# Kernel optimization log

Hardware: AMD Instinct MI355X
Metric: run time of the kernel (lower is better)

The kernel has to match this reference:

```python
import jax, jax.numpy as jnp
import numpy as np

H, W, C = 56, 56, 384
WS, SHIFT, HEADS = 7, 3, 12
HEAD_DIM = C // HEADS
SCALE = HEAD_DIM ** (-0.5)
NWIN = (H // WS) * (W // WS)  # 64 windows per image
NTOK = WS * WS                # 49 tokens per window
EPS = 1e-5


def _gen_mask():
    # static shift-window attention mask, computed with numpy (jit-safe constant)
    img = np.zeros((H, W))
    sl = (slice(0, -WS), slice(-WS, -SHIFT), slice(-SHIFT, None))
    cnt = 0
    for hs in sl:
        for ws in sl:
            img[hs, ws] = cnt
            cnt += 1
    mw = img.reshape(H // WS, WS, W // WS, WS).transpose(0, 2, 1, 3).reshape(-1, NTOK)
    diff = mw[:, None, :] - mw[:, :, None]  # (NWIN, NTOK, NTOK)
    return jnp.asarray(np.where(diff != 0, -100.0, 0.0), dtype=jnp.float32)

ATTN_MASK = _gen_mask()


def _layernorm(x, g, b):
    mu = jnp.mean(x, axis=-1, keepdims=True)
    var = jnp.var(x, axis=-1, keepdims=True)
    return (x - mu) * jax.lax.rsqrt(var + EPS) * g + b


def setup_inputs() -> dict:
    key = jax.random.key(0)
    ks = jax.random.split(key, 6)
    s = 0.02
    return {
        "x": jax.random.normal(ks[0], (16, H * W, C), dtype=jnp.float32),
        "ln1_g": jnp.ones((C,), jnp.float32),
        "ln1_b": jnp.zeros((C,), jnp.float32),
        "qkv_w": jax.random.normal(ks[1], (C, 3 * C), jnp.float32) * s,
        "proj_w": jax.random.normal(ks[2], (C, C), jnp.float32) * s,
        "proj_b": jnp.zeros((C,), jnp.float32),
        "ln2_g": jnp.ones((C,), jnp.float32),
        "ln2_b": jnp.zeros((C,), jnp.float32),
        "fc1_w": jax.random.normal(ks[3], (C, 4 * C), jnp.float32) * s,
        "fc1_b": jnp.zeros((4 * C,), jnp.float32),
        "fc2_w": jax.random.normal(ks[4], (4 * C, C), jnp.float32) * s,
        "fc2_b": jnp.zeros((C,), jnp.float32),
    }


def reference(x, ln1_g, ln1_b, qkv_w, proj_w, proj_b, ln2_g, ln2_b, fc1_w, fc1_b, fc2_w, fc2_b):
    B, N, _ = x.shape
    h = x
    y = _layernorm(x, ln1_g, ln1_b).reshape(B, H, W, C)
    # cyclic shift (note: source never rolls back; we match it)
    y = jnp.roll(y, shift=(-SHIFT, -SHIFT), axis=(1, 2))
    # window partition -> (B*NWIN, NTOK, C)
    y = y.reshape(B, H // WS, WS, W // WS, WS, C).transpose(0, 1, 3, 2, 4, 5)
    y = y.reshape(B * NWIN, NTOK, C)
    # qkv (no bias), split heads
    qkv = (y @ qkv_w).reshape(B * NWIN, NTOK, 3, HEADS, HEAD_DIM)
    qkv = qkv.transpose(2, 0, 3, 1, 4)  # (3, BW, heads, NTOK, hd)
    q, k, v = qkv[0], qkv[1], qkv[2]
    attn = jnp.einsum('whnd,whmd->whnm', q, k) * SCALE  # (BW, heads, NTOK, NTOK)
    attn = attn.reshape(B, NWIN, HEADS, NTOK, NTOK) + ATTN_MASK[None, :, None]
    attn = jax.nn.softmax(attn.reshape(B * NWIN, HEADS, NTOK, NTOK), axis=-1)
    o = jnp.einsum('whnm,whmd->whnd', attn, v)
    o = o.transpose(0, 2, 1, 3).reshape(B * NWIN, NTOK, C)
    o = o @ proj_w + proj_b
    # window reverse -> (B, N, C)
    o = o.reshape(B, H // WS, W // WS, WS, WS, C).transpose(0, 1, 3, 2, 4, 5)
    o = o.reshape(B, N, C)
    x1 = h + o
    # MLP (GELU after both fc1 and fc2, as in source)
    m = _layernorm(x1, ln2_g, ln2_b)
    m = jax.nn.gelu(m @ fc1_w + fc1_b, approximate=False)
    m = jax.nn.gelu(m @ fc2_w + fc2_b, approximate=False)
    return x1 + m
```

## Files before the change

### kernel.cpp

```cpp
#include <hip/hip_runtime.h>
#include <hip/hip_bf16.h>
#include <cstdint>
#include <cstddef>

#define C_DIM   384
#define NIMG    3136
#define MROWS   50176
#define QK_SCALE 0.17677669529663687f

using bf16x8 = __attribute__((ext_vector_type(8))) short;
using f32x4  = __attribute__((ext_vector_type(4))) float;

__device__ __forceinline__ short f2bf(float f) {
  union { float f; uint32_t u; } v; v.f = f;
  uint32_t r = (v.u + 0x7fffu + ((v.u >> 16) & 1u)) >> 16;
  return (short)(uint16_t)r;
}

__device__ __forceinline__ float bf2f(short s) {
  union { uint32_t u; float f; } v; v.u = ((uint32_t)(uint16_t)s) << 16;
  return v.f;
}

__device__ __forceinline__ void async_copy16(const void* g, void* l) {
  __builtin_amdgcn_global_load_lds(
      (const __attribute__((address_space(1))) void*)g,
      (__attribute__((address_space(3))) void*)l, 16, 0, 0);
}

__device__ __forceinline__ float gelu_fast(float x) {
  float x2 = x * x;
  float u = fmaf(0.0356774081f, x2, 0.7978845608f);
  float e = exp2f(x * u * 2.8853900818f);
  float r = __builtin_amdgcn_rcpf(e + 1.0f);
  return fmaf(-x, r, x);
}

__global__ __launch_bounds__(256) void transpose_cast(
    const float* __restrict__ w, short* __restrict__ wt, int K, int N) {
  int idx = blockIdx.x * 256 + threadIdx.x;
  if (idx >= K * N) return;
  int k = idx / N;
  int n = idx - k * N;
  wt[(size_t)n * K + k] = f2bf(w[idx]);
}

template <typename IN>
__global__ __launch_bounds__(256) void ln_kernel(
    const IN* __restrict__ x, const float* __restrict__ g,
    const float* __restrict__ b, short* __restrict__ y, int windowed) {
  int token = blockIdx.x * 4 + (threadIdx.x >> 6);
  int lane = threadIdx.x & 63;
  size_t src;
  if (windowed) {
    int bw = token / 49;
    int tt = token - bw * 49;
    int bb = bw >> 6, w = bw & 63;
    int hs = (w >> 3) * 7 + tt / 7 + 3; if (hs >= 56) hs -= 56;
    int ws = (w & 7) * 7 + (tt % 7) + 3; if (ws >= 56) ws -= 56;
    src = (size_t)(bb * NIMG + hs * 56 + ws) * C_DIM;
  } else {
    src = (size_t)token * C_DIM;
  }
  const IN* xr = x + src;
  float v[6];
  float s = 0.f;
#pragma unroll
  for (int i = 0; i < 6; ++i) {
    if constexpr (sizeof(IN) == 4) v[i] = (float)xr[lane + i * 64];
    else v[i] = bf2f((short)xr[lane + i * 64]);
    s += v[i];
  }
#pragma unroll
  for (int m = 1; m < 64; m <<= 1) s += __shfl_xor(s, m);
  float mu = s * (1.0f / 384.0f);
  float var = 0.f;
#pragma unroll
  for (int i = 0; i < 6; ++i) { float d = v[i] - mu; var += d * d; }
#pragma unroll
  for (int m = 1; m < 64; m <<= 1) var += __shfl_xor(var, m);
  float rstd = rsqrtf(var * (1.0f / 384.0f) + 1e-5f);
  short* yr = y + (size_t)token * C_DIM;
#pragma unroll
  for (int i = 0; i < 6; ++i) {
    int c = lane + i * 64;
    yr[c] = f2bf((v[i] - mu) * rstd * g[c] + b[c]);
  }
}

template <int EPI>
__device__ __forceinline__ void gemm_epilogue(
    f32x4 (&acc)[4][4], void* Out, const float* bias, const void* resid,
    int N, int m0, int n0, int wm, int wn, int lrow, int quad) {
#pragma unroll
  for (int i = 0; i < 4; ++i) {
#pragma unroll
    for (int r = 0; r < 4; ++r) {
      int row = m0 + wm * 64 + i * 16 + quad * 4 + r;
      if (EPI == 1) {
        int bw = row / 49;
        int tt = row - bw * 49;
        int bb = bw >> 6, w = bw & 63;
        int nimg = ((w >> 3) * 7 + tt / 7) * 56 + (w & 7) * 7 + (tt % 7);
        size_t obase = ((size_t)(bb * NIMG + nimg)) * C_DIM;
#pragma unroll
        for (int j = 0; j < 4; ++j) {
          int col = n0 + wn * 64 + j * 16 + lrow;
          size_t oi = obase + col;
          ((short*)Out)[oi] =
              f2bf(acc[i][j][r] + bias[col] + ((const float*)resid)[oi]);
        }
      } else {
#pragma unroll
        for (int j = 0; j < 4; ++j) {
          int col = n0 + wn * 64 + j * 16 + lrow;
          float v = acc[i][j][r];
          if (EPI == 0) {
            ((short*)Out)[(size_t)row * N + col] = f2bf(v);
          } else if (EPI == 2) {
            ((short*)Out)[(size_t)row * N + col] = f2bf(gelu_fast(v + bias[col]));
          } else {
            size_t oi = (size_t)row * C_DIM + col;
            ((float*)Out)[oi] =
                bf2f(((const short*)resid)[oi]) + gelu_fast(v + bias[col]);
          }
        }
      }
    }
  }
}

__device__ __forceinline__ void grid_decode(int nby, int& m0, int& n0) {
  const int wg = (int)blockIdx.x;
  const int swz = (wg & 7) * ((int)gridDim.x >> 3) + (wg >> 3);
  const int mb = swz / nby;
  const int nb = swz - mb * nby;
  m0 = mb * 128;
  n0 = nb * 128;
}

template <int EPI>
__global__ __launch_bounds__(256, 4) void gemm_kernel(
    const short* __restrict__ A, const short* __restrict__ Bt,
    void* __restrict__ Out, const float* __restrict__ bias,
    const void* __restrict__ resid, int M, int N, int K, int nby) {
  __shared__ __align__(16) short lds[128 * 64 * 2];
  const int t = threadIdx.x;
  const int wave = t >> 6, lane = t & 63;
  const int lrow = lane & 15, quad = lane >> 4;
  const int wm = wave & 1, wn = wave >> 1;
  int m0, n0;
  grid_decode(nby, m0, n0);

  f32x4 acc[4][4] = {};
  const int srow = t >> 3;
  const int spos = t & 7;
  const int nt = K >> 6;
  short* ldsA = lds;
  short* ldsB = lds + 128 * 64;

  for (int kt = 0; kt < nt; ++kt) {
    int k0 = kt * 64;
    __syncthreads();
#pragma unroll
    for (int i = 0; i < 4; ++i) {
      int row = i * 32 + srow;
      int ca = spos ^ (row & 7);
      async_copy16(A + (size_t)(m0 + row) * K + k0 + ca * 8,
                   ldsA + (i * 32 + wave * 8) * 64);
      async_copy16(Bt + (size_t)(n0 + row) * K + k0 + ca * 8,
                   ldsB + (i * 32 + wave * 8) * 64);
    }
    __syncthreads();
#pragma unroll
    for (int ks = 0; ks < 2; ++ks) {
      const int cb = ks * 4;
      bf16x8 af[4], bfr[4];
#pragma unroll
      for (int i = 0; i < 4; ++i) {
        int ra = wm * 64 + i * 16 + lrow;
        af[i] = *(const bf16x8*)(ldsA + ra * 64 + (((cb + quad) ^ (ra & 7)) * 8));
        int rb = wn * 64 + i * 16 + lrow;
        bfr[i] = *(const bf16x8*)(ldsB + rb * 64 + (((cb + quad) ^ (rb & 7)) * 8));
      }
#pragma unroll
      for (int i = 0; i < 4; ++i)
#pragma unroll
        for (int j = 0; j < 4; ++j)
          acc[i][j] = __builtin_amdgcn_mfma_f32_16x16x32_bf16(af[i], bfr[j],
                                                              acc[i][j], 0, 0, 0);
    }
  }
  gemm_epilogue<EPI>(acc, Out, bias, resid, N, m0, n0, wm, wn, lrow, quad);
}

template <int EPI>
__global__ __launch_bounds__(256, 3) void gemm_pipe_kernel(
    const short* __restrict__ A, const short* __restrict__ Bt,
    void* __restrict__ Out, const float* __restrict__ bias,
    const void* __restrict__ resid, int M, int N, int K, int nby) {
  __shared__ __align__(16) short lds[3][128 * 32 * 2];
  const int t = threadIdx.x;
  const int wave = t >> 6, lane = t & 63;
  const int lrow = lane & 15, quad = lane >> 4;
  const int wm = wave & 1, wn = wave >> 1;
  int m0, n0;
  grid_decode(nby, m0, n0);

  f32x4 acc[4][4] = {};
  const int srow = t >> 2;
  const int spos = t & 3;
  const int nt = K >> 5;

  auto stage = [&](int buf, int k0) {
    short* la = &lds[buf][0];
    short* lb = la + 128 * 32;
#pragma unroll
    for (int i = 0; i < 2; ++i) {
      int row = i * 64 + srow;
      int ca = spos ^ (row & 3);
      async_copy16(A + (size_t)(m0 + row) * K + k0 + ca * 8,
                   la + (i * 64 + wave * 16) * 32);
      async_copy16(Bt + (size_t)(n0 + row) * K + k0 + ca * 8,
                   lb + (i * 64 + wave * 16) * 32);
    }
  };

  auto compute = [&](int buf) {
    short* ldsA = &lds[buf][0];
    short* ldsB = ldsA + 128 * 32;
    bf16x8 af[4], bfr[4];
#pragma unroll
    for (int i = 0; i < 4; ++i) {
      int ra = wm * 64 + i * 16 + lrow;
      af[i] = *(const bf16x8*)(ldsA + ra * 32 + ((quad ^ (ra & 3)) * 8));
      int rb = wn * 64 + i * 16 + lrow;
      bfr[i] = *(const bf16x8*)(ldsB + rb * 32 + ((quad ^ (rb & 3)) * 8));
    }
    __builtin_amdgcn_s_setprio(1);
#pragma unroll
    for (int i = 0; i < 4; ++i)
#pragma unroll
      for (int j = 0; j < 4; ++j)
        acc[i][j] = __builtin_amdgcn_mfma_f32_16x16x32_bf16(af[i], bfr[j],
                                                            acc[i][j], 0, 0, 0);
    __builtin_amdgcn_s_setprio(0);
  };

  stage(0, 0);
  stage(1, 32);
  int cbuf = 0, sbuf = 2;
  for (int kt = 0; kt < nt; ++kt) {
    __builtin_amdgcn_sched_barrier(0);
    if (kt + 2 < nt) {
      stage(sbuf, (kt + 2) * 32);
      asm volatile("s_waitcnt vmcnt(8)" ::: "memory");
    } else if (kt + 1 < nt) {
      asm volatile("s_waitcnt vmcnt(4)" ::: "memory");
    } else {
      asm volatile("s_waitcnt vmcnt(0)" ::: "memory");
    }
    __builtin_amdgcn_s_barrier();
    __builtin_amdgcn_sched_barrier(0);
    compute(cbuf);
    __builtin_amdgcn_sched_barrier(0);
    __builtin_amdgcn_s_barrier();
    cbuf = (cbuf == 2) ? 0 : cbuf + 1;
    sbuf = (sbuf == 2) ? 0 : sbuf + 1;
  }
  gemm_epilogue<EPI>(acc, Out, bias, resid, N, m0, n0, wm, wn, lrow, quad);
}

__global__ __launch_bounds__(256) void attn_kernel(
    const short* __restrict__ qkv, short* __restrict__ o) {
  __shared__ __align__(16) short plds[4][64 * 72];
  const int wavei = threadIdx.x >> 6;
  const int lane = threadIdx.x & 63;
  const int gw = blockIdx.x * 4 + wavei;
  const int bw = gw / 12;
  const int h = gw - bw * 12;
  const int w = bw & 63;
  const int lrow = lane & 15, quad = lane >> 4;
  const short* base = qkv + (size_t)bw * 49 * 1152 + h * 32;

  bf16x8 qf[4], kf[4];
#pragma unroll
  for (int i = 0; i < 4; ++i) {
    int tq = i * 16 + lrow;
    const short* p = base + (size_t)tq * 1152 + quad * 8;
    qf[i] = *(const bf16x8*)p;
    kf[i] = *(const bf16x8*)(p + 384);
  }
  f32x4 sa[4][4] = {};
#pragma unroll
  for (int i = 0; i < 4; ++i)
#pragma unroll
    for (int j = 0; j < 4; ++j)
      sa[i][j] = __builtin_amdgcn_mfma_f32_16x16x32_bf16(qf[i], kf[j], sa[i][j], 0, 0, 0);

  int tl = lane < 49 ? lane : 0;
  int rr = tl / 7, cc = tl - rr * 7;
  int hs = (w >> 3) * 7 + rr;
  int ws = (w & 7) * 7 + cc;
  int id = (hs < 49 ? 0 : (hs < 53 ? 3 : 6)) + (ws < 49 ? 0 : (ws < 53 ? 1 : 2));

  int idn[4], idm[4][4];
#pragma unroll
  for (int j = 0; j < 4; ++j) idn[j] = __shfl(id, j * 16 + lrow);
#pragma unroll
  for (int i = 0; i < 4; ++i)
#pragma unroll
    for (int r = 0; r < 4; ++r) idm[i][r] = __shfl(id, i * 16 + quad * 4 + r);

#pragma unroll
  for (int i = 0; i < 4; ++i)
#pragma unroll
    for (int j = 0; j < 4; ++j)
#pragma unroll
      for (int r = 0; r < 4; ++r) {
        float v = sa[i][j][r] * QK_SCALE + (idm[i][r] == idn[j] ? 0.f : -100.f);
        sa[i][j][r] = (j * 16 + lrow < 49) ? v : -1e30f;
      }

#pragma unroll
  for (int i = 0; i < 4; ++i)
#pragma unroll
    for (int r = 0; r < 4; ++r) {
      float mx = -1e30f;
#pragma unroll
      for (int j = 0; j < 4; ++j) mx = fmaxf(mx, sa[i][j][r]);
#pragma unroll
      for (int m = 1; m < 16; m <<= 1) mx = fmaxf(mx, __shfl_xor(mx, m));
      float sum = 0.f;
#pragma unroll
      for (int j = 0; j < 4; ++j) {
        float e = exp2f((sa[i][j][r] - mx) * 1.44269504f);
        sa[i][j][r] = e;
        sum += e;
      }
#pragma unroll
      for (int m = 1; m < 16; m <<= 1) sum += __shfl_xor(sum, m);
      float inv = 1.0f / sum;
#pragma unroll
      for (int j = 0; j < 4; ++j) sa[i][j][r] *= inv;
    }

  short* pw = plds[wavei];
#pragma unroll
  for (int i = 0; i < 4; ++i)
#pragma unroll
    for (int r = 0; r < 4; ++r)
#pragma unroll
      for (int j = 0; j < 4; ++j)
        pw[(i * 16 + quad * 4 + r) * 72 + j * 16 + lrow] = f2bf(sa[i][j][r]);

  f32x4 oa[4][2] = {};
#pragma unroll
  for (int kk = 0; kk < 2; ++kk) {
    bf16x8 vf[2];
#pragma unroll
    for (int j2 = 0; j2 < 2; ++j2) {
#pragma unroll
      for (int jj = 0; jj < 8; ++jj) {
        int n = kk * 32 + quad * 8 + jj;
        vf[j2][jj] = (n < 49)
            ? base[768 + (size_t)n * 1152 + j2 * 16 + lrow]
            : (short)0;
      }
    }
#pragma unroll
    for (int i = 0; i < 4; ++i) {
      bf16x8 pf = *(const bf16x8*)(pw + (i * 16 + lrow) * 72 + kk * 32 + quad * 8);
#pragma unroll
      for (int j2 = 0; j2 < 2; ++j2)
        oa[i][j2] = __builtin_amdgcn_mfma_f32_16x16x32_bf16(pf, vf[j2], oa[i][j2], 0, 0, 0);
    }
  }

#pragma unroll
  for (int i = 0; i < 4; ++i)
#pragma unroll
    for (int j2 = 0; j2 < 2; ++j2)
#pragma unroll
      for (int r = 0; r < 4; ++r) {
        int m = i * 16 + quad * 4 + r;
        if (m < 49)
          o[((size_t)bw * 49 + m) * 384 + h * 32 + j2 * 16 + lrow] = f2bf(oa[i][j2][r]);
      }
}

extern "C" void kernel_launch(void* const* d_in, const int* in_sizes, int n_in,
                              void* d_out, int out_size, void* d_ws, size_t ws_size,
                              hipStream_t stream) {
  const float* x      = (const float*)d_in[0];
  const float* ln1_g  = (const float*)d_in[1];
  const float* ln1_b  = (const float*)d_in[2];
  const float* qkv_w  = (const float*)d_in[3];
  const float* proj_w = (const float*)d_in[4];
  const float* proj_b = (const float*)d_in[5];
  const float* ln2_g  = (const float*)d_in[6];
  const float* ln2_b  = (const float*)d_in[7];
  const float* fc1_w  = (const float*)d_in[8];
  const float* fc1_b  = (const float*)d_in[9];
  const float* fc2_w  = (const float*)d_in[10];
  const float* fc2_b  = (const float*)d_in[11];
  float* out = (float*)d_out;

  char* ws = (char*)d_ws;
  auto alloc = [&](size_t bytes) {
    char* p = ws;
    ws += (bytes + 255) & ~(size_t)255;
    return p;
  };
  short* qkv_wT  = (short*)alloc((size_t)1152 * 384 * 2);
  short* proj_wT = (short*)alloc((size_t)384 * 384 * 2);
  short* fc1_wT  = (short*)alloc((size_t)1536 * 384 * 2);
  short* fc2_wT  = (short*)alloc((size_t)384 * 1536 * 2);
  short* bufA    = (short*)alloc((size_t)MROWS * 384 * 2);
  short* x1      = (short*)alloc((size_t)MROWS * 384 * 2);
  short* bufB    = (short*)alloc((size_t)MROWS * 1536 * 2);

  transpose_cast<<<(384 * 1152) / 256, 256, 0, stream>>>(qkv_w, qkv_wT, 384, 1152);
  transpose_cast<<<(384 * 384) / 256, 256, 0, stream>>>(proj_w, proj_wT, 384, 384);
  transpose_cast<<<(384 * 1536) / 256, 256, 0, stream>>>(fc1_w, fc1_wT, 384, 1536);
  transpose_cast<<<(1536 * 384) / 256, 256, 0, stream>>>(fc2_w, fc2_wT, 1536, 384);

  ln_kernel<float><<<MROWS / 4, 256, 0, stream>>>(x, ln1_g, ln1_b, bufA, 1);

  gemm_kernel<0><<<392 * 9, 256, 0, stream>>>(bufA, qkv_wT, bufB, nullptr,
                                              nullptr, MROWS, 1152, 384, 9);

  attn_kernel<<<3072, 256, 0, stream>>>(bufB, bufA);

  gemm_kernel<1><<<392 * 3, 256, 0, stream>>>(bufA, proj_wT, x1, proj_b,
                                              x, MROWS, 384, 384, 3);

  ln_kernel<short><<<MROWS / 4, 256, 0, stream>>>(x1, ln2_g, ln2_b, bufA, 0);

  gemm_kernel<2><<<392 * 12, 256, 0, stream>>>(bufA, fc1_wT, bufB, fc1_b,
                                               nullptr, MROWS, 1536, 384, 12);

  gemm_pipe_kernel<3><<<392 * 3, 256, 0, stream>>>(bufB, fc2_wT, out, fc2_b,
                                                   x1, MROWS, 384, 1536, 3);
}
```

Baseline: 517.1 us.

## Double-buffer K=384 GEMMs with BK=32 prefetch and switch fc2 to BK=64

The single-buffered K=384 GEMM (qkv, proj, fc1) becomes a double-buffered BK=32 pipeline. It prefetches the next K tile while MFMA runs on the current one, and uses a modified XOR swizzle ((row>>1)&3) to limit LDS bank conflicts. The fc2 GEMM (K=1536) moves from a triple-buffered BK=32 pipeline to a double-buffered BK=64 pipeline with occupancy hint 2. The aim is to hide global load latency and cut barriers per K step. In exchange it uses more LDS per block and may lower occupancy.

```diff
diff --git a/kernel.cpp b/kernel.cpp
--- a/kernel.cpp
+++ b/kernel.cpp
@@ -140,11 +140,11 @@
 }
 
 template <int EPI>
-__global__ __launch_bounds__(256, 4) void gemm_kernel(
+__global__ __launch_bounds__(256, 4) void gemm_pipe32_kernel(
     const short* __restrict__ A, const short* __restrict__ Bt,
     void* __restrict__ Out, const float* __restrict__ bias,
     const void* __restrict__ resid, int M, int N, int K, int nby) {
-  __shared__ __align__(16) short lds[128 * 64 * 2];
+  __shared__ __align__(16) short lds[2][128 * 32 * 2];
   const int t = threadIdx.x;
   const int wave = t >> 6, lane = t & 63;
   const int lrow = lane & 15, quad = lane >> 4;
@@ -153,53 +153,69 @@
   grid_decode(nby, m0, n0);
 
   f32x4 acc[4][4] = {};
-  const int srow = t >> 3;
-  const int spos = t & 7;
-  const int nt = K >> 6;
-  short* ldsA = lds;
-  short* ldsB = lds + 128 * 64;
-
+  const int srow = t >> 2;
+  const int spos = t & 3;
+  const int nt = K >> 5;
+
+  auto stage = [&](int buf, int k0) {
+    short* la = &lds[buf][0];
+    short* lb = la + 128 * 32;
+#pragma unroll
+    for (int i = 0; i < 2; ++i) {
+      int row = i * 64 + srow;
+      int ca = spos ^ ((row >> 1) & 3);
+      async_copy16(A + (size_t)(m0 + row) * K + k0 + ca * 8,
+                   la + (i * 64 + wave * 16) * 32);
+      async_copy16(Bt + (size_t)(n0 + row) * K + k0 + ca * 8,
+                   lb + (i * 64 + wave * 16) * 32);
+    }
+  };
+
+  auto compute = [&](int buf) {
+    short* ldsA = &lds[buf][0];
+    short* ldsB = ldsA + 128 * 32;
+    bf16x8 af[4], bfr[4];
+#pragma unroll
+    for (int i = 0; i < 4; ++i) {
+      int ra = wm * 64 + i * 16 + lrow;
+      af[i] = *(const bf16x8*)(ldsA + ra * 32 + ((quad ^ ((ra >> 1) & 3)) * 8));
+      int rb = wn * 64 + i * 16 + lrow;
+      bfr[i] = *(const bf16x8*)(ldsB + rb * 32 + ((quad ^ ((rb >> 1) & 3)) * 8));
+    }
+    __builtin_amdgcn_s_setprio(1);
+#pragma unroll
+    for (int i = 0; i < 4; ++i)
+#pragma unroll
+      for (int j = 0; j < 4; ++j)
+        acc[i][j] = __builtin_amdgcn_mfma_f32_16x16x32_bf16(af[i], bfr[j],
+                                                            acc[i][j], 0, 0, 0);
+    __builtin_amdgcn_s_setprio(0);
+  };
+
+  stage(0, 0);
   for (int kt = 0; kt < nt; ++kt) {
-    int k0 = kt * 64;
-    __syncthreads();
-#pragma unroll
-    for (int i = 0; i < 4; ++i) {
-      int row = i * 32 + srow;
-      int ca = spos ^ (row & 7);
-      async_copy16(A + (size_t)(m0 + row) * K + k0 + ca * 8,
-                   ldsA + (i * 32 + wave * 8) * 64);
-      async_copy16(Bt + (size_t)(n0 + row) * K + k0 + ca * 8,
-                   ldsB + (i * 32 + wave * 8) * 64);
-    }
-    __syncthreads();
-#pragma unroll
-    for (int ks = 0; ks < 2; ++ks) {
-      const int cb = ks * 4;
-      bf16x8 af[4], bfr[4];
-#pragma unroll
-      for (int i = 0; i < 4; ++i) {
-        int ra = wm * 64 + i * 16 + lrow;
-        af[i] = *(const bf16x8*)(ldsA + ra * 64 + (((cb + quad) ^ (ra & 7)) * 8));
-        int rb = wn * 64 + i * 16 + lrow;
-        bfr[i] = *(const bf16x8*)(ldsB + rb * 64 + (((cb + quad) ^ (rb & 7)) * 8));
-      }
-#pragma unroll
-      for (int i = 0; i < 4; ++i)
-#pragma unroll
-        for (int j = 0; j < 4; ++j)
-          acc[i][j] = __builtin_amdgcn_mfma_f32_16x16x32_bf16(af[i], bfr[j],
-                                                              acc[i][j], 0, 0, 0);
-    }
+    __builtin_amdgcn_sched_barrier(0);
+    if (kt + 1 < nt) {
+      stage((kt + 1) & 1, (kt + 1) * 32);
+      asm volatile("s_waitcnt vmcnt(4)" ::: "memory");
+    } else {
+      asm volatile("s_waitcnt vmcnt(0)" ::: "memory");
+    }
+    __builtin_amdgcn_s_barrier();
+    __builtin_amdgcn_sched_barrier(0);
+    compute(kt & 1);
+    __builtin_amdgcn_sched_barrier(0);
+    __builtin_amdgcn_s_barrier();
   }
   gemm_epilogue<EPI>(acc, Out, bias, resid, N, m0, n0, wm, wn, lrow, quad);
 }
 
 template <int EPI>
-__global__ __launch_bounds__(256, 3) void gemm_pipe_kernel(
+__global__ __launch_bounds__(256, 2) void gemm_pipe64_kernel(
     const short* __restrict__ A, const short* __restrict__ Bt,
     void* __restrict__ Out, const float* __restrict__ bias,
     const void* __restrict__ resid, int M, int N, int K, int nby) {
-  __shared__ __align__(16) short lds[3][128 * 32 * 2];
+  __shared__ __align__(16) short lds[2][128 * 64 * 2];
   const int t = threadIdx.x;
   const int wave = t >> 6, lane = t & 63;
   const int lrow = lane & 15, quad = lane >> 4;
@@ -208,65 +224,63 @@
   grid_decode(nby, m0, n0);
 
   f32x4 acc[4][4] = {};
-  const int srow = t >> 2;
-  const int spos = t & 3;
-  const int nt = K >> 5;
+  const int srow = t >> 3;
+  const int spos = t & 7;
+  const int nt = K >> 6;
 
   auto stage = [&](int buf, int k0) {
     short* la = &lds[buf][0];
-    short* lb = la + 128 * 32;
-#pragma unroll
-    for (int i = 0; i < 2; ++i) {
-      int row = i * 64 + srow;
-      int ca = spos ^ (row & 3);
+    short* lb = la + 128 * 64;
+#pragma unroll
+    for (int i = 0; i < 4; ++i) {
+      int row = i * 32 + srow;
+      int ca = spos ^ (row & 7);
       async_copy16(A + (size_t)(m0 + row) * K + k0 + ca * 8,
-                   la + (i * 64 + wave * 16) * 32);
+                   la + (i * 32 + wave * 8) * 64);
       async_copy16(Bt + (size_t)(n0 + row) * K + k0 + ca * 8,
-                   lb + (i * 64 + wave * 16) * 32);
+                   lb + (i * 32 + wave * 8) * 64);
     }
   };
 
   auto compute = [&](int buf) {
     short* ldsA = &lds[buf][0];
-    short* ldsB = ldsA + 128 * 32;
-    bf16x8 af[4], bfr[4];
-#pragma unroll
-    for (int i = 0; i < 4; ++i) {
-      int ra = wm * 64 + i * 16 + lrow;
-      af[i] = *(const bf16x8*)(ldsA + ra * 32 + ((quad ^ (ra & 3)) * 8));
-      int rb = wn * 64 + i * 16 + lrow;
-      bfr[i] = *(const bf16x8*)(ldsB + rb * 32 + ((quad ^ (rb & 3)) * 8));
-    }
-    __builtin_amdgcn_s_setprio(1);
-#pragma unroll
-    for (int i = 0; i < 4; ++i)
-#pragma unroll
-      for (int j = 0; j < 4; ++j)
-        acc[i][j] = __builtin_amdgcn_mfma_f32_16x16x32_bf16(af[i], bfr[j],
-                                                            acc[i][j], 0, 0, 0);
-    __builtin_amdgcn_s_setprio(0);
+    short* ldsB = ldsA + 128 * 64;
+#pragma unroll
+    for (int ks = 0; ks < 2; ++ks) {
+      const int cb = ks * 4;
+      bf16x8 af[4], bfr[4];
+#pragma unroll
+      for (int i = 0; i < 4; ++i) {
+        int ra = wm * 64 + i * 16 + lrow;
+        af[i] = *(const bf16x8*)(ldsA + ra * 64 + (((cb + quad) ^ (ra & 7)) * 8));
+        int rb = wn * 64 + i * 16 + lrow;
+        bfr[i] = *(const bf16x8*)(ldsB + rb * 64 + (((cb + quad) ^ (rb & 7)) * 8));
+      }
+      __builtin_amdgcn_s_setprio(1);
+#pragma unroll
+      for (int i = 0; i < 4; ++i)
+#pragma unroll
+        for (int j = 0; j < 4; ++j)
+          acc[i][j] = __builtin_amdgcn_mfma_f32_16x16x32_bf16(af[i], bfr[j],
+                                                              acc[i][j], 0, 0, 0);
+      __builtin_amdgcn_s_setprio(0);
+    }
   };
 
   stage(0, 0);
-  stage(1, 32);
-  int cbuf = 0, sbuf = 2;
   for (int kt = 0; kt < nt; ++kt) {
     __builtin_amdgcn_sched_barrier(0);
-    if (kt + 2 < nt) {
-      stage(sbuf, (kt + 2) * 32);
+    if (kt + 1 < nt) {
+      stage((kt + 1) & 1, (kt + 1) * 64);
       asm volatile("s_waitcnt vmcnt(8)" ::: "memory");
-    } else if (kt + 1 < nt) {
-      asm volatile("s_waitcnt vmcnt(4)" ::: "memory");
     } else {
       asm volatile("s_waitcnt vmcnt(0)" ::: "memory");
     }
     __builtin_amdgcn_s_barrier();
     __builtin_amdgcn_sched_barrier(0);
-    compute(cbuf);
+    compute(kt & 1);
     __builtin_amdgcn_sched_barrier(0);
     __builtin_amdgcn_s_barrier();
-    cbuf = (cbuf == 2) ? 0 : cbuf + 1;
-    sbuf = (sbuf == 2) ? 0 : sbuf + 1;
   }
   gemm_epilogue<EPI>(acc, Out, bias, resid, N, m0, n0, wm, wn, lrow, quad);
 }
@@ -427,19 +441,19 @@
 
   ln_kernel<float><<<MROWS / 4, 256, 0, stream>>>(x, ln1_g, ln1_b, bufA, 1);
 
-  gemm_kernel<0><<<392 * 9, 256, 0, stream>>>(bufA, qkv_wT, bufB, nullptr,
-                                              nullptr, MROWS, 1152, 384, 9);
+  gemm_pipe32_kernel<0><<<392 * 9, 256, 0, stream>>>(bufA, qkv_wT, bufB, nullptr,
+                                                     nullptr, MROWS, 1152, 384, 9);
 
   attn_kernel<<<3072, 256, 0, stream>>>(bufB, bufA);
 
-  gemm_kernel<1><<<392 * 3, 256, 0, stream>>>(bufA, proj_wT, x1, proj_b,
-                                              x, MROWS, 384, 384, 3);
+  gemm_pipe32_kernel<1><<<392 * 3, 256, 0, stream>>>(bufA, proj_wT, x1, proj_b,
+                                                     x, MROWS, 384, 384, 3);
 
   ln_kernel<short><<<MROWS / 4, 256, 0, stream>>>(x1, ln2_g, ln2_b, bufA, 0);
 
-  gemm_kernel<2><<<392 * 12, 256, 0, stream>>>(bufA, fc1_wT, bufB, fc1_b,
-                                               nullptr, MROWS, 1536, 384, 12);
-
-  gemm_pipe_kernel<3><<<392 * 3, 256, 0, stream>>>(bufB, fc2_wT, out, fc2_b,
-                                                   x1, MROWS, 384, 1536, 3);
-}
+  gemm_pipe32_kernel<2><<<392 * 12, 256, 0, stream>>>(bufA, fc1_wT, bufB, fc1_b,
+                                                      nullptr, MROWS, 1536, 384, 12);
+
+  gemm_pipe64_kernel<3><<<392 * 3, 256, 0, stream>>>(bufB, fc2_wT, out, fc2_b,
+                                                     x1, MROWS, 384, 1536, 3);
+}
```

Result: no change. 519.7 us (+0.5%).
